# Kernel tuning notes

Hardware: AMD Instinct MI355X
Metric: run time of the kernel (lower is better)

Reference implementation:

```python
import jax, jax.numpy as jnp
import numpy as np

GROUPS = 8
EPS = 1e-3  # keras GroupNormalization default epsilon


def group_norm(x, gamma, beta):
    # x: [B, H, W, C], channels-last, normalize over (H, W, C//G) per group
    B, H, W, C = x.shape
    g = x.reshape(B, H, W, GROUPS, C // GROUPS)
    mean = g.mean(axis=(1, 2, 4), keepdims=True)
    var = g.var(axis=(1, 2, 4), keepdims=True)
    g = (g - mean) * jax.lax.rsqrt(var + EPS)
    return g.reshape(B, H, W, C) * gamma + beta


def setup_inputs() -> dict:
    key = jax.random.key(0)
    ks = jax.random.split(key, 6)
    B, H, W, C = 4, 64, 64, 256
    s = 1.0 / np.sqrt(C)
    return {
        "x": jax.random.normal(ks[0], (B, H, W, C), jnp.float32),
        "gn_gamma": jnp.ones((C,), jnp.float32),
        "gn_beta": jnp.zeros((C,), jnp.float32),
        "Wq": jax.random.normal(ks[1], (C, C), jnp.float32) * s,
        "bq": jnp.zeros((C,), jnp.float32),
        "Wk": jax.random.normal(ks[2], (C, C), jnp.float32) * s,
        "bk": jnp.zeros((C,), jnp.float32),
        "Wv": jax.random.normal(ks[3], (C, C), jnp.float32) * s,
        "bv": jnp.zeros((C,), jnp.float32),
        "Wp": jax.random.normal(ks[4], (C, C), jnp.float32) * s,
        "bp": jnp.zeros((C,), jnp.float32),
    }


def reference(x, gn_gamma, gn_beta, Wq, bq, Wk, bk, Wv, bv, Wp, bp):
    B, H, W, C = x.shape
    scale = jnp.float32(C) ** -0.5
    xn = group_norm(x, gn_gamma, gn_beta)  # note: residual uses NORMALIZED input (as in source)
    xf = xn.reshape(B, H * W, C)           # flatten spatial -> [B, N, C]
    q = xf @ Wq + bq
    k = xf @ Wk + bk
    v = xf @ Wv + bv
    attn = jnp.einsum('bnc,bmc->bnm', q, k) * scale  # [B, N, N]
    attn = jax.nn.softmax(attn, axis=-1)
    out = jnp.einsum('bnm,bmc->bnc', attn, v)
    out = out @ Wp + bp
    return xn + out.reshape(B, H, W, C)
```

## Files before the change

### kernel.cpp

```cpp
#include <hip/hip_runtime.h>
#include <hip/hip_bf16.h>

typedef __bf16 bf16x8 __attribute__((ext_vector_type(8)));
typedef __bf16 bf16x4 __attribute__((ext_vector_type(4)));
typedef float f32x4 __attribute__((ext_vector_type(4)));
typedef float f32x16 __attribute__((ext_vector_type(16)));

#define MFMA16(a,b,c) __builtin_amdgcn_mfma_f32_16x16x32_bf16((a),(b),(c),0,0,0)
#define MFMA32(a,b,c) __builtin_amdgcn_mfma_f32_32x32x16_bf16((a),(b),(c),0,0,0)

__device__ __forceinline__ void gload_lds16(const void* g, void* l) {
    __builtin_amdgcn_global_load_lds((const __attribute__((address_space(1))) unsigned int*)g,
                                     (__attribute__((address_space(3))) unsigned int*)l, 16, 0, 0);
}

__global__ __launch_bounds__(256) void gn_stats1(const float* __restrict__ x,
                                                 float* __restrict__ pstats) {
    int blk = blockIdx.x;
    int bg = blk >> 4, sl = blk & 15;
    int b = bg >> 3, g = bg & 7;
    const float* base = x + ((size_t)b * 4096 + sl * 256) * 256 + g * 32;
    float s = 0.f, s2 = 0.f;
    for (int i = threadIdx.x; i < 2048; i += 256) {
        int pos = i >> 3, f4 = i & 7;
        float4 v = *(const float4*)(base + (size_t)pos * 256 + f4 * 4);
        s  += v.x + v.y + v.z + v.w;
        s2 += v.x * v.x + v.y * v.y + v.z * v.z + v.w * v.w;
    }
    for (int off = 32; off; off >>= 1) {
        s  += __shfl_down(s, off);
        s2 += __shfl_down(s2, off);
    }
    __shared__ float red[8];
    int wave = threadIdx.x >> 6, lane = threadIdx.x & 63;
    if (lane == 0) { red[wave] = s; red[4 + wave] = s2; }
    __syncthreads();
    if (threadIdx.x == 0) {
        pstats[blk * 2]     = red[0] + red[1] + red[2] + red[3];
        pstats[blk * 2 + 1] = red[4] + red[5] + red[6] + red[7];
    }
}

__global__ void gn_stats2(const float* __restrict__ pstats, float* __restrict__ stats) {
    int bg = threadIdx.x;
    if (bg < 32) {
        float S = 0.f, S2 = 0.f;
        for (int sl = 0; sl < 16; sl++) {
            S  += pstats[(bg * 16 + sl) * 2];
            S2 += pstats[(bg * 16 + sl) * 2 + 1];
        }
        const float invN = 1.f / 131072.f;
        float mean = S * invN;
        float var = S2 * invN - mean * mean;
        stats[bg * 2] = mean;
        stats[bg * 2 + 1] = rsqrtf(var + 1e-3f);
    }
}

__global__ __launch_bounds__(256) void gn_norm(const float* __restrict__ x,
                                               const float* __restrict__ gamma,
                                               const float* __restrict__ beta,
                                               const float* __restrict__ stats,
                                               float* __restrict__ xn_f32,
                                               __bf16* __restrict__ xn_bf) {
    size_t idx = (size_t)blockIdx.x * 256 + threadIdx.x;
    int c4 = (int)(idx & 63);
    int row = (int)(idx >> 6);
    int b = row >> 12;
    int g = c4 >> 3;
    float mean = stats[(b * 8 + g) * 2];
    float rstd = stats[(b * 8 + g) * 2 + 1];
    float4 xv = ((const float4*)x)[idx];
    float4 ga = ((const float4*)gamma)[c4];
    float4 be = ((const float4*)beta)[c4];
    float4 r;
    r.x = (xv.x - mean) * rstd * ga.x + be.x;
    r.y = (xv.y - mean) * rstd * ga.y + be.y;
    r.z = (xv.z - mean) * rstd * ga.z + be.z;
    r.w = (xv.w - mean) * rstd * ga.w + be.w;
    ((float4*)xn_f32)[idx] = r;
    bf16x4 o;
    o[0] = (__bf16)r.x; o[1] = (__bf16)r.y; o[2] = (__bf16)r.z; o[3] = (__bf16)r.w;
    *(bf16x4*)(xn_bf + idx * 4) = o;
}

__global__ __launch_bounds__(256) void prep_w(const float* __restrict__ Wq,
                                              const float* __restrict__ Wk,
                                              const float* __restrict__ Wv,
                                              const float* __restrict__ Wp,
                                              __bf16* __restrict__ wt) {
    int o = blockIdx.x * 256 + threadIdx.x;
    int w = o >> 16;
    int rem = o & 65535;
    int nt   = rem >> 12;
    int kf   = (rem >> 9) & 7;
    int quad = (rem >> 7) & 3;
    int l16  = (rem >> 3) & 15;
    int j    = rem & 7;
    int n = nt * 16 + l16;
    int k = kf * 32 + quad * 8 + j;
    const float* W = (w == 0) ? Wq : (w == 1) ? Wk : (w == 2) ? Wv : Wp;
    wt[o] = (__bf16)W[k * 256 + n];
}

__global__ __launch_bounds__(128, 2) void qkv_gemm(const __bf16* __restrict__ xn,
                                                   const __bf16* __restrict__ wt,
                                                   const float* __restrict__ bq,
                                                   const float* __restrict__ bk,
                                                   const float* __restrict__ bv,
                                                   __bf16* __restrict__ qout,
                                                   __bf16* __restrict__ kout,
                                                   __bf16* __restrict__ vtout) {
    __shared__ __bf16 atile[64][264];
    int w = blockIdx.z;
    const __bf16* Wl = wt + (size_t)w * 65536;
    int tid = threadIdx.x;
    int wave = tid >> 6, lane = tid & 63;
    int quad = lane >> 4, l16 = lane & 15;
    int m0 = blockIdx.x * 64;
    int ntbase = blockIdx.y * 8 + wave * 4;

#pragma unroll
    for (int i = 0; i < 16; i++) {
        int c = tid + 128 * i;
        int row = c >> 5, col = (c & 31) * 8;
        *(bf16x8*)&atile[row][col] = *(const bf16x8*)(xn + (size_t)(m0 + row) * 256 + col);
    }
    bf16x8 bfr[4][8];
#pragma unroll
    for (int ct = 0; ct < 4; ct++)
#pragma unroll
        for (int kf = 0; kf < 8; kf++)
            bfr[ct][kf] = *(const bf16x8*)(Wl + ((((size_t)(ntbase + ct) * 8 + kf) * 4 + quad) * 16 + l16) * 8);
    __syncthreads();

    f32x4 acc[4][4];
#pragma unroll
    for (int mt = 0; mt < 4; mt++)
#pragma unroll
        for (int ct = 0; ct < 4; ct++)
#pragma unroll
            for (int r = 0; r < 4; r++) acc[mt][ct][r] = 0.f;
#pragma unroll
    for (int kf = 0; kf < 8; kf++) {
        bf16x8 af[4];
#pragma unroll
        for (int mt = 0; mt < 4; mt++)
            af[mt] = *(const bf16x8*)&atile[mt * 16 + l16][kf * 32 + quad * 8];
#pragma unroll
        for (int mt = 0; mt < 4; mt++)
#pragma unroll
            for (int ct = 0; ct < 4; ct++)
                acc[mt][ct] = MFMA16(af[mt], bfr[ct][kf], acc[mt][ct]);
    }
    const float* bias = (w == 0) ? bq : (w == 1) ? bk : bv;
#pragma unroll
    for (int mt = 0; mt < 4; mt++) {
#pragma unroll
        for (int ct = 0; ct < 4; ct++) {
            int c = (ntbase + ct) * 16 + l16;
            float bias_v = bias[c];
#pragma unroll
            for (int r = 0; r < 4; r++) {
                int m = m0 + mt * 16 + quad * 4 + r;
                float val = acc[mt][ct][r] + bias_v;
                if (w == 2) {
                    int bb = m >> 12, n = m & 4095;
                    vtout[((size_t)(bb * 256 + c)) * 4096 + n] = (__bf16)val;
                } else if (w == 0) {
                    qout[(size_t)m * 256 + c] = (__bf16)(val * 0.0625f);
                } else {
                    kout[(size_t)m * 256 + c] = (__bf16)val;
                }
            }
        }
    }
}

__global__ __launch_bounds__(256, 2) void flash_attn(const __bf16* __restrict__ q,
                                                     const __bf16* __restrict__ k,
                                                     const __bf16* __restrict__ vt,
                                                     __bf16* __restrict__ po,
                                                     float* __restrict__ ml) {
    __shared__ __align__(16) char smem[69632];
    __bf16 (*vtile0)[36] = (__bf16(*)[36])(smem + 32768);
    __bf16 (*vtile1)[36] = (__bf16(*)[36])(smem + 51200);
    __bf16 (*otr)[32][264] = (__bf16(*)[32][264])smem;

    const int tid = threadIdx.x;
    const int wave = tid >> 6, lane = tid & 63;
    const int l32 = lane & 31, h = lane >> 5;
    const int qt = blockIdx.x, ks = blockIdx.y, b = blockIdx.z;
    const int row0 = qt * 128 + wave * 32;
    const size_t rowg0 = (size_t)b * 4096 + row0;

    const char*   kb = (const char*)(k + ((size_t)b * 4096 + ks * 1024) * 256);
    const __bf16* vb = vt + (size_t)b * 256 * 4096 + ks * 1024;

    int koff[4];
#pragma unroll
    for (int i = 0; i < 4; i++) {
        int P = wave * 256 + i * 64 + lane;
        int r = P >> 5, cp = P & 31;
        koff[i] = r * 512 + (cp ^ r) * 16;
    }
    const int kldsoff = wave * 4096;

    bf16x8 qf[16];
    const __bf16* qbase = q + (rowg0 + l32) * 256 + h * 8;
#pragma unroll
    for (int s = 0; s < 16; s++) qf[s] = *(const bf16x8*)(qbase + s * 16);

    f32x16 acc[8];
#pragma unroll
    for (int ct = 0; ct < 8; ct++)
#pragma unroll
        for (int r = 0; r < 16; r++) acc[ct][r] = 0.f;
    float mi = -1e30f, li = 0.f;

    const int vr_ = tid >> 2, vc4 = tid & 3;

#pragma unroll
    for (int i = 0; i < 4; i++)
        gload_lds16(kb + koff[i], smem + kldsoff + i * 1024);
    {
        bf16x8 vc[4];
#pragma unroll
        for (int i = 0; i < 4; i++)
            vc[i] = *(const bf16x8*)(vb + (size_t)(vr_ + 64 * i) * 4096 + vc4 * 8);
#pragma unroll
        for (int i = 0; i < 4; i++)
            *(bf16x8*)&vtile0[vr_ + 64 * i][vc4 * 8] = vc[i];
    }
    __syncthreads();

    for (int it = 0; it < 32; ++it) {
        const int cur = it & 1;
        char* kcur = smem + (cur ? 16384 : 0);
        char* knxt = smem + (cur ? 0 : 16384);
        __bf16 (*vcur)[36] = cur ? vtile1 : vtile0;
        __bf16 (*vnxt)[36] = cur ? vtile0 : vtile1;

        bf16x8 vc[4];
        if (it + 1 < 32) {
            const char* kg = kb + (size_t)(it + 1) * 16384;
#pragma unroll
            for (int i = 0; i < 4; i++)
                gload_lds16(kg + koff[i], knxt + kldsoff + i * 1024);
            const int kn = (it + 1) * 32;
#pragma unroll
            for (int i = 0; i < 4; i++)
                vc[i] = *(const bf16x8*)(vb + (size_t)(vr_ + 64 * i) * 4096 + kn + vc4 * 8);
        }

        f32x16 s;
#pragma unroll
        for (int r = 0; r < 16; r++) s[r] = 0.f;
#pragma unroll
        for (int kf = 0; kf < 16; kf++) {
            int cl = kf * 2 + h;
            bf16x8 ka = *(const bf16x8*)(kcur + l32 * 512 + ((cl ^ l32) << 4));
            s = MFMA32(ka, qf[kf], s);
        }
        float mx = s[0];
#pragma unroll
        for (int r = 1; r < 16; r++) mx = fmaxf(mx, s[r]);
        mx = fmaxf(mx, __shfl_xor(mx, 32));
        float mnew = fmaxf(mi, mx);
        float alpha = __expf(mi - mnew);
        float rs = 0.f;
#pragma unroll
        for (int r = 0; r < 16; r++) { float p = __expf(s[r] - mnew); s[r] = p; rs += p; }
        rs += __shfl_xor(rs, 32);
        li = li * alpha + rs;
        bool need = (mnew > mi);
        mi = mnew;
        bf16x8 pf0, pf1;
#pragma unroll
        for (int j = 0; j < 8; j++) { pf0[j] = (__bf16)s[j]; pf1[j] = (__bf16)s[8 + j]; }
        if (__ballot(need)) {
#pragma unroll
            for (int ct = 0; ct < 8; ct++)
#pragma unroll
                for (int r = 0; r < 16; r++) acc[ct][r] *= alpha;
        }
        if (it + 1 < 32) {
#pragma unroll
            for (int i = 0; i < 4; i++)
                *(bf16x8*)&vnxt[vr_ + 64 * i][vc4 * 8] = vc[i];
        }
#pragma unroll
        for (int ct = 0; ct < 8; ct++) {
            const __bf16* vr = &vcur[ct * 32 + l32][0];
            bf16x4 a00 = *(const bf16x4*)(vr + 4 * h);
            bf16x4 a01 = *(const bf16x4*)(vr + 8 + 4 * h);
            bf16x8 va0 = __builtin_shufflevector(a00, a01, 0, 1, 2, 3, 4, 5, 6, 7);
            acc[ct] = MFMA32(va0, pf0, acc[ct]);
            bf16x4 a10 = *(const bf16x4*)(vr + 16 + 4 * h);
            bf16x4 a11 = *(const bf16x4*)(vr + 24 + 4 * h);
            bf16x8 va1 = __builtin_shufflevector(a10, a11, 0, 1, 2, 3, 4, 5, 6, 7);
            acc[ct] = MFMA32(va1, pf1, acc[ct]);
        }
        __syncthreads();
    }

#pragma unroll
    for (int ct = 0; ct < 8; ct++) {
#pragma unroll
        for (int pk = 0; pk < 4; pk++) {
            bf16x4 op;
            op[0] = (__bf16)acc[ct][pk * 4];     op[1] = (__bf16)acc[ct][pk * 4 + 1];
            op[2] = (__bf16)acc[ct][pk * 4 + 2]; op[3] = (__bf16)acc[ct][pk * 4 + 3];
            *(bf16x4*)&otr[wave][l32][ct * 32 + pk * 8 + h * 4] = op;
        }
    }
    if (lane < 32) {
        float2 v; v.x = mi; v.y = li;
        *(float2*)&ml[((size_t)ks * 16384 + rowg0 + l32) * 2] = v;
    }
    __syncthreads();
    __bf16* pobase = po + ((size_t)ks * 16384 + rowg0) * 256;
    const int rr = lane >> 1, half = lane & 1;
#pragma unroll
    for (int j = 0; j < 16; j++) {
        bf16x8 val = *(const bf16x8*)&otr[wave][rr][half * 128 + j * 8];
        *(bf16x8*)(pobase + (size_t)rr * 256 + half * 128 + j * 8) = val;
    }
}

__global__ __launch_bounds__(256) void merge_attn(const __bf16* __restrict__ po,
                                                  const float* __restrict__ ml,
                                                  __bf16* __restrict__ ao) {
    int t = blockIdx.x * 256 + threadIdx.x;
    int row = t >> 5, c8 = t & 31;
    float mm[4], ll[4];
#pragma unroll
    for (int s = 0; s < 4; s++) {
        float2 v = *(const float2*)&ml[((size_t)s * 16384 + row) * 2];
        mm[s] = v.x; ll[s] = v.y;
    }
    float M = fmaxf(fmaxf(mm[0], mm[1]), fmaxf(mm[2], mm[3]));
    float den = 0.f, w[4];
#pragma unroll
    for (int s = 0; s < 4; s++) { w[s] = __expf(mm[s] - M); den += ll[s] * w[s]; }
    float accv[8];
#pragma unroll
    for (int e = 0; e < 8; e++) accv[e] = 0.f;
#pragma unroll
    for (int s = 0; s < 4; s++) {
        bf16x8 pv = *(const bf16x8*)(po + ((size_t)s * 16384 + row) * 256 + c8 * 8);
#pragma unroll
        for (int e = 0; e < 8; e++) accv[e] += w[s] * (float)pv[e];
    }
    float rinv = 1.f / den;
    bf16x8 o;
#pragma unroll
    for (int e = 0; e < 8; e++) o[e] = (__bf16)(accv[e] * rinv);
    *(bf16x8*)(ao + (size_t)row * 256 + c8 * 8) = o;
}

__global__ __launch_bounds__(128, 2) void proj_gemm(const __bf16* __restrict__ ao,
                                                    const __bf16* __restrict__ wpl,
                                                    const float* __restrict__ bp,
                                                    float* __restrict__ out) {
    __shared__ __bf16 atile[64][264];
    int tid = threadIdx.x;
    int wave = tid >> 6, lane = tid & 63;
    int quad = lane >> 4, l16 = lane & 15;
    int m0 = blockIdx.x * 64;
    int ntbase = blockIdx.y * 8 + wave * 4;

#pragma unroll
    for (int i = 0; i < 16; i++) {
        int c = tid + 128 * i;
        int row = c >> 5, col = (c & 31) * 8;
        *(bf16x8*)&atile[row][col] = *(const bf16x8*)(ao + (size_t)(m0 + row) * 256 + col);
    }
    bf16x8 bfr[4][8];
#pragma unroll
    for (int ct = 0; ct < 4; ct++)
#pragma unroll
        for (int kf = 0; kf < 8; kf++)
            bfr[ct][kf] = *(const bf16x8*)(wpl + ((((size_t)(ntbase + ct) * 8 + kf) * 4 + quad) * 16 + l16) * 8);
    __syncthreads();

    f32x4 acc[4][4];
#pragma unroll
    for (int mt = 0; mt < 4; mt++)
#pragma unroll
        for (int ct = 0; ct < 4; ct++)
#pragma unroll
            for (int r = 0; r < 4; r++) acc[mt][ct][r] = 0.f;
#pragma unroll
    for (int kf = 0; kf < 8; kf++) {
        bf16x8 af[4];
#pragma unroll
        for (int mt = 0; mt < 4; mt++)
            af[mt] = *(const bf16x8*)&atile[mt * 16 + l16][kf * 32 + quad * 8];
#pragma unroll
        for (int mt = 0; mt < 4; mt++)
#pragma unroll
            for (int ct = 0; ct < 4; ct++)
                acc[mt][ct] = MFMA16(af[mt], bfr[ct][kf], acc[mt][ct]);
    }
#pragma unroll
    for (int mt = 0; mt < 4; mt++) {
#pragma unroll
        for (int ct = 0; ct < 4; ct++) {
            int c = (ntbase + ct) * 16 + l16;
            float bias_v = bp[c];
#pragma unroll
            for (int r = 0; r < 4; r++) {
                int m = m0 + mt * 16 + quad * 4 + r;
                size_t idx = (size_t)m * 256 + c;
                out[idx] = out[idx] + acc[mt][ct][r] + bias_v;
            }
        }
    }
}

extern "C" void kernel_launch(void* const* d_in, const int* in_sizes, int n_in,
                              void* d_out, int out_size, void* d_ws, size_t ws_size,
                              hipStream_t stream) {
    const float* x     = (const float*)d_in[0];
    const float* gamma = (const float*)d_in[1];
    const float* beta  = (const float*)d_in[2];
    const float* Wq    = (const float*)d_in[3];
    const float* bq    = (const float*)d_in[4];
    const float* Wk    = (const float*)d_in[5];
    const float* bk    = (const float*)d_in[6];
    const float* Wv    = (const float*)d_in[7];
    const float* bv    = (const float*)d_in[8];
    const float* Wp    = (const float*)d_in[9];
    const float* bp    = (const float*)d_in[10];
    float* out = (float*)d_out;

    char* ws = (char*)d_ws;
    __bf16* xn_bf   = (__bf16*)(ws);
    __bf16* wt      = (__bf16*)(ws + 8388608);
    __bf16* qbuf    = (__bf16*)(ws + 8912896);
    __bf16* kbuf    = (__bf16*)(ws + 17301504);
    __bf16* vtbuf   = (__bf16*)(ws + 25690112);
    __bf16* po      = (__bf16*)(ws + 34078720);
    float*  ml      = (float*)(ws + 67633152);
    float*  pstats  = (float*)(ws + 68157440);
    float*  gstats  = (float*)(ws + 68161536);
    __bf16* aobuf   = qbuf;

    gn_stats1<<<512, 256, 0, stream>>>(x, pstats);
    gn_stats2<<<1, 64, 0, stream>>>(pstats, gstats);
    gn_norm<<<4096, 256, 0, stream>>>(x, gamma, beta, gstats, out, xn_bf);
    prep_w<<<1024, 256, 0, stream>>>(Wq, Wk, Wv, Wp, wt);
    qkv_gemm<<<dim3(256, 2, 3), 128, 0, stream>>>(xn_bf, wt, bq, bk, bv, qbuf, kbuf, vtbuf);
    flash_attn<<<dim3(32, 4, 4), 256, 0, stream>>>(qbuf, kbuf, vtbuf, po, ml);
    merge_attn<<<2048, 256, 0, stream>>>(po, ml, aobuf);
    proj_gemm<<<dim3(256, 2), 128, 0, stream>>>(aobuf, wt + 3 * 65536, bp, out);
}
```

Measured before the change: 265.4 us.

## Fuse attention merge into projection GEMM, stage V-transpose stores, use exp2 softmax

The qkv_gemm V path now transposes its output through LDS so it writes coalesced 16-byte rows instead of scattered 2-byte stores. Q is prescaled by log2(e)/sqrt(C) so flash attention can use exp2f. The V tile is stored in an interleaved layout so each P·V MFMA operand becomes one 16-byte LDS read, and that store is moved earlier in the loop. The separate merge_attn kernel is removed and its split-KV combine now runs inside proj_gemm's A-tile load. This saves one launch and one round trip of the merged output, but each proj_gemm block recomputes the merge for its rows (duplicated across the two y-blocks).

```diff
diff --git a/kernel.cpp b/kernel.cpp
--- a/kernel.cpp
+++ b/kernel.cpp
@@ -153,24 +153,46 @@
             for (int ct = 0; ct < 4; ct++)
                 acc[mt][ct] = MFMA16(af[mt], bfr[ct][kf], acc[mt][ct]);
     }
-    const float* bias = (w == 0) ? bq : (w == 1) ? bk : bv;
-#pragma unroll
-    for (int mt = 0; mt < 4; mt++) {
-#pragma unroll
-        for (int ct = 0; ct < 4; ct++) {
-            int c = (ntbase + ct) * 16 + l16;
-            float bias_v = bias[c];
-#pragma unroll
-            for (int r = 0; r < 4; r++) {
-                int m = m0 + mt * 16 + quad * 4 + r;
-                float val = acc[mt][ct][r] + bias_v;
-                if (w == 2) {
-                    int bb = m >> 12, n = m & 4095;
-                    vtout[((size_t)(bb * 256 + c)) * 4096 + n] = (__bf16)val;
-                } else if (w == 0) {
-                    qout[(size_t)m * 256 + c] = (__bf16)(val * 0.0625f);
-                } else {
-                    kout[(size_t)m * 256 + c] = (__bf16)val;
+
+    if (w == 2) {
+        __syncthreads();
+        __bf16 (*vtl)[70] = (__bf16(*)[70])atile;
+#pragma unroll
+        for (int mt = 0; mt < 4; mt++) {
+#pragma unroll
+            for (int ct = 0; ct < 4; ct++) {
+                int cl = (wave * 4 + ct) * 16 + l16;
+                float bias_v = bv[blockIdx.y * 128 + cl];
+                bf16x4 pv;
+#pragma unroll
+                for (int r = 0; r < 4; r++) pv[r] = (__bf16)(acc[mt][ct][r] + bias_v);
+                *(bf16x4*)&vtl[cl][mt * 16 + quad * 4] = pv;
+            }
+        }
+        __syncthreads();
+        int bb = m0 >> 12, n0g = m0 & 4095;
+#pragma unroll
+        for (int j = 0; j < 8; j++) {
+            int chunk = tid + 128 * j;
+            int cl = chunk >> 3, n8 = chunk & 7;
+            *(bf16x8*)(vtout + ((size_t)(bb * 256 + blockIdx.y * 128 + cl)) * 4096 + n0g + n8 * 8)
+                = *(const bf16x8*)&vtl[cl][n8 * 8];
+        }
+    } else {
+        const float* bias = (w == 0) ? bq : bk;
+        const float qscale = 0.09016844f;
+#pragma unroll
+        for (int mt = 0; mt < 4; mt++) {
+#pragma unroll
+            for (int ct = 0; ct < 4; ct++) {
+                int c = (ntbase + ct) * 16 + l16;
+                float bias_v = bias[c];
+#pragma unroll
+                for (int r = 0; r < 4; r++) {
+                    int m = m0 + mt * 16 + quad * 4 + r;
+                    float val = acc[mt][ct][r] + bias_v;
+                    if (w == 0) qout[(size_t)m * 256 + c] = (__bf16)(val * qscale);
+                    else        kout[(size_t)m * 256 + c] = (__bf16)val;
                 }
             }
         }
@@ -219,6 +241,7 @@
     float mi = -1e30f, li = 0.f;
 
     const int vr_ = tid >> 2, vc4 = tid & 3;
+    const int vbase = 16 * (vc4 >> 1) + 4 * (vc4 & 1);
 
 #pragma unroll
     for (int i = 0; i < 4; i++)
@@ -229,8 +252,12 @@
         for (int i = 0; i < 4; i++)
             vc[i] = *(const bf16x8*)(vb + (size_t)(vr_ + 64 * i) * 4096 + vc4 * 8);
 #pragma unroll
-        for (int i = 0; i < 4; i++)
-            *(bf16x8*)&vtile0[vr_ + 64 * i][vc4 * 8] = vc[i];
+        for (int i = 0; i < 4; i++) {
+            bf16x4 lo = __builtin_shufflevector(vc[i], vc[i], 0, 1, 2, 3);
+            bf16x4 hi = __builtin_shufflevector(vc[i], vc[i], 4, 5, 6, 7);
+            *(bf16x4*)&vtile0[vr_ + 64 * i][vbase]     = lo;
+            *(bf16x4*)&vtile0[vr_ + 64 * i][vbase + 8] = hi;
+        }
     }
     __syncthreads();
 
@@ -262,15 +289,26 @@
             bf16x8 ka = *(const bf16x8*)(kcur + l32 * 512 + ((cl ^ l32) << 4));
             s = MFMA32(ka, qf[kf], s);
         }
+
+        if (it + 1 < 32) {
+#pragma unroll
+            for (int i = 0; i < 4; i++) {
+                bf16x4 lo = __builtin_shufflevector(vc[i], vc[i], 0, 1, 2, 3);
+                bf16x4 hi = __builtin_shufflevector(vc[i], vc[i], 4, 5, 6, 7);
+                *(bf16x4*)&vnxt[vr_ + 64 * i][vbase]     = lo;
+                *(bf16x4*)&vnxt[vr_ + 64 * i][vbase + 8] = hi;
+            }
+        }
+
         float mx = s[0];
 #pragma unroll
         for (int r = 1; r < 16; r++) mx = fmaxf(mx, s[r]);
         mx = fmaxf(mx, __shfl_xor(mx, 32));
         float mnew = fmaxf(mi, mx);
-        float alpha = __expf(mi - mnew);
+        float alpha = exp2f(mi - mnew);
         float rs = 0.f;
 #pragma unroll
-        for (int r = 0; r < 16; r++) { float p = __expf(s[r] - mnew); s[r] = p; rs += p; }
+        for (int r = 0; r < 16; r++) { float p = exp2f(s[r] - mnew); s[r] = p; rs += p; }
         rs += __shfl_xor(rs, 32);
         li = li * alpha + rs;
         bool need = (mnew > mi);
@@ -284,21 +322,13 @@
 #pragma unroll
                 for (int r = 0; r < 16; r++) acc[ct][r] *= alpha;
         }
-        if (it + 1 < 32) {
-#pragma unroll
-            for (int i = 0; i < 4; i++)
-                *(bf16x8*)&vnxt[vr_ + 64 * i][vc4 * 8] = vc[i];
-        }
+
 #pragma unroll
         for (int ct = 0; ct < 8; ct++) {
             const __bf16* vr = &vcur[ct * 32 + l32][0];
-            bf16x4 a00 = *(const bf16x4*)(vr + 4 * h);
-            bf16x4 a01 = *(const bf16x4*)(vr + 8 + 4 * h);
-            bf16x8 va0 = __builtin_shufflevector(a00, a01, 0, 1, 2, 3, 4, 5, 6, 7);
+            bf16x8 va0 = *(const bf16x8*)(vr + 8 * h);
             acc[ct] = MFMA32(va0, pf0, acc[ct]);
-            bf16x4 a10 = *(const bf16x4*)(vr + 16 + 4 * h);
-            bf16x4 a11 = *(const bf16x4*)(vr + 24 + 4 * h);
-            bf16x8 va1 = __builtin_shufflevector(a10, a11, 0, 1, 2, 3, 4, 5, 6, 7);
+            bf16x8 va1 = *(const bf16x8*)(vr + 16 + 8 * h);
             acc[ct] = MFMA32(va1, pf1, acc[ct]);
         }
         __syncthreads();
@@ -328,38 +358,8 @@
     }
 }
 
-__global__ __launch_bounds__(256) void merge_attn(const __bf16* __restrict__ po,
-                                                  const float* __restrict__ ml,
-                                                  __bf16* __restrict__ ao) {
-    int t = blockIdx.x * 256 + threadIdx.x;
-    int row = t >> 5, c8 = t & 31;
-    float mm[4], ll[4];
-#pragma unroll
-    for (int s = 0; s < 4; s++) {
-        float2 v = *(const float2*)&ml[((size_t)s * 16384 + row) * 2];
-        mm[s] = v.x; ll[s] = v.y;
-    }
-    float M = fmaxf(fmaxf(mm[0], mm[1]), fmaxf(mm[2], mm[3]));
-    float den = 0.f, w[4];
-#pragma unroll
-    for (int s = 0; s < 4; s++) { w[s] = __expf(mm[s] - M); den += ll[s] * w[s]; }
-    float accv[8];
-#pragma unroll
-    for (int e = 0; e < 8; e++) accv[e] = 0.f;
-#pragma unroll
-    for (int s = 0; s < 4; s++) {
-        bf16x8 pv = *(const bf16x8*)(po + ((size_t)s * 16384 + row) * 256 + c8 * 8);
-#pragma unroll
-        for (int e = 0; e < 8; e++) accv[e] += w[s] * (float)pv[e];
-    }
-    float rinv = 1.f / den;
-    bf16x8 o;
-#pragma unroll
-    for (int e = 0; e < 8; e++) o[e] = (__bf16)(accv[e] * rinv);
-    *(bf16x8*)(ao + (size_t)row * 256 + c8 * 8) = o;
-}
-
-__global__ __launch_bounds__(128, 2) void proj_gemm(const __bf16* __restrict__ ao,
+__global__ __launch_bounds__(128, 2) void proj_gemm(const __bf16* __restrict__ po,
+                                                    const float* __restrict__ ml,
                                                     const __bf16* __restrict__ wpl,
                                                     const float* __restrict__ bp,
                                                     float* __restrict__ out) {
@@ -373,8 +373,32 @@
 #pragma unroll
     for (int i = 0; i < 16; i++) {
         int c = tid + 128 * i;
-        int row = c >> 5, col = (c & 31) * 8;
-        *(bf16x8*)&atile[row][col] = *(const bf16x8*)(ao + (size_t)(m0 + row) * 256 + col);
+        int row = c >> 5, col8 = c & 31;
+        int m = m0 + row;
+        float mm[4], ll[4];
+#pragma unroll
+        for (int s = 0; s < 4; s++) {
+            float2 v = *(const float2*)&ml[((size_t)s * 16384 + m) * 2];
+            mm[s] = v.x; ll[s] = v.y;
+        }
+        float M = fmaxf(fmaxf(mm[0], mm[1]), fmaxf(mm[2], mm[3]));
+        float den = 0.f, w[4];
+#pragma unroll
+        for (int s = 0; s < 4; s++) { w[s] = exp2f(mm[s] - M); den += ll[s] * w[s]; }
+        float accv[8];
+#pragma unroll
+        for (int e = 0; e < 8; e++) accv[e] = 0.f;
+#pragma unroll
+        for (int s = 0; s < 4; s++) {
+            bf16x8 pv = *(const bf16x8*)(po + ((size_t)s * 16384 + m) * 256 + col8 * 8);
+#pragma unroll
+            for (int e = 0; e < 8; e++) accv[e] += w[s] * (float)pv[e];
+        }
+        float rinv = 1.f / den;
+        bf16x8 o;
+#pragma unroll
+        for (int e = 0; e < 8; e++) o[e] = (__bf16)(accv[e] * rinv);
+        *(bf16x8*)&atile[row][col8 * 8] = o;
     }
     bf16x8 bfr[4][8];
 #pragma unroll
@@ -445,7 +469,6 @@
     float*  ml      = (float*)(ws + 67633152);
     float*  pstats  = (float*)(ws + 68157440);
     float*  gstats  = (float*)(ws + 68161536);
-    __bf16* aobuf   = qbuf;
 
     gn_stats1<<<512, 256, 0, stream>>>(x, pstats);
     gn_stats2<<<1, 64, 0, stream>>>(pstats, gstats);
@@ -453,6 +476,5 @@
     prep_w<<<1024, 256, 0, stream>>>(Wq, Wk, Wv, Wp, wt);
     qkv_gemm<<<dim3(256, 2, 3), 128, 0, stream>>>(xn_bf, wt, bq, bk, bv, qbuf, kbuf, vtbuf);
     flash_attn<<<dim3(32, 4, 4), 256, 0, stream>>>(qbuf, kbuf, vtbuf, po, ml);
-    merge_attn<<<2048, 256, 0, stream>>>(po, ml, aobuf);
-    proj_gemm<<<dim3(256, 2), 128, 0, stream>>>(aobuf, wt + 3 * 65536, bp, out);
-}
+    proj_gemm<<<dim3(256, 2), 128, 0, stream>>>(po, ml, wt + 3 * 65536, bp, out);
+}
```

Result: slower. 319.7 us (+20.5%).
